# Performance work log

Hardware: AMD Instinct MI355X
Metric: run time of the kernel (lower is better)

## Reference

```python
import jax, jax.numpy as jnp
import numpy as np

N_NODES = 50000
N_EDGES = 1000000
IN_C = 128
HID_C = 128
N_REL = 8


def rgcn_conv(x, W, root, b, src, dst, et, n_rel):
    # PyG-style RGCNConv: per-relation linear transform of source features,
    # mean-aggregated per (target node, relation), plus root transform + bias.
    n = x.shape[0]
    h = jnp.einsum('nd,rdh->nrh', x, W)          # [N, R, H] per-relation transforms
    msgs = h[src, et]                            # [E, H] gather per-edge message
    seg = dst * n_rel + et                       # combined (node, relation) segment id
    agg = jax.ops.segment_sum(msgs, seg, num_segments=n * n_rel)        # [N*R, H]
    cnt = jax.ops.segment_sum(jnp.ones_like(msgs[:, 0]), seg, num_segments=n * n_rel)
    agg = agg / jnp.maximum(cnt, 1.0)[:, None]   # mean over edges of each relation
    return agg.reshape(n, n_rel, -1).sum(axis=1) + x @ root + b


def setup_inputs() -> dict:
    key = jax.random.key(0)
    ks = jax.random.split(key, 12)
    s = 1.0 / np.sqrt(IN_C)
    sh = 1.0 / np.sqrt(HID_C)
    return {
        'x': jax.random.normal(ks[0], (N_NODES, IN_C), dtype=jnp.float32),
        'ei': jax.random.randint(ks[1], (2, N_EDGES), 0, N_NODES, dtype=jnp.int32),
        'et': jax.random.randint(ks[2], (N_EDGES,), 0, N_REL, dtype=jnp.int32),
        'W1': jax.random.normal(ks[3], (N_REL, IN_C, HID_C), dtype=jnp.float32) * s,
        'root1': jax.random.normal(ks[4], (IN_C, HID_C), dtype=jnp.float32) * s,
        'b1': jnp.zeros((HID_C,), dtype=jnp.float32),
        'W2': jax.random.normal(ks[5], (N_REL, HID_C, HID_C), dtype=jnp.float32) * sh,
        'root2': jax.random.normal(ks[6], (HID_C, HID_C), dtype=jnp.float32) * sh,
        'b2': jnp.zeros((HID_C,), dtype=jnp.float32),
        'lin_W': jax.random.normal(ks[7], (HID_C, HID_C), dtype=jnp.float32) * sh,
        'lin_b': jnp.zeros((HID_C,), dtype=jnp.float32),
    }


def reference(x, ei, et, W1, root1, b1, W2, root2, b2, lin_W, lin_b):
    src, dst = ei[0], ei[1]
    h = jax.nn.relu(rgcn_conv(x, W1, root1, b1, src, dst, et, N_REL))
    h = rgcn_conv(h, W2, root2, b2, src, dst, et, N_REL)
    return h @ lin_W + lin_b
```

## Files before the change

kernel.cpp:

```cpp
#include <hip/hip_runtime.h>
#include <hip/hip_bf16.h>

#define N_NODES 50000
#define N_EDGES 1000000
#define C       128
#define N_REL   8
#define N_SEG   (N_NODES * N_REL)
#define KTOT    (N_REL * C + C)
#define KC_CNT  (KTOT / 32)
#define A_STRIDE 1160
#define NCHUNK  ((N_SEG + 1023) / 1024)
#define MV_N    (N_SEG + 1 + N_EDGES)
#define NBLK    (N_NODES / 16)
#define FE_BLK  ((N_EDGES + 511) / 512)

typedef __hip_bfloat16  bf16;
typedef __hip_bfloat162 bf162;
typedef __attribute__((ext_vector_type(8))) short short8;
typedef __attribute__((ext_vector_type(4))) float f32x4;
typedef __attribute__((ext_vector_type(2))) float f32x2;

__device__ __forceinline__ size_t frag_index(int k, int n) {
    int nt = n >> 4, n15 = n & 15;
    int kc = k >> 5, quad = (k >> 3) & 3, j = k & 7;
    int lane = quad * 16 + n15;
    return ((size_t)(nt * KC_CNT + kc) * 64 + lane) * 8 + j;
}

#define CVT_BLOCKS ((N_NODES * C / 2) / 256)
#define CNT_BLOCKS ((N_EDGES + 255) / 256)
__global__ void prep_kernel(const float2* __restrict__ xf, unsigned int* __restrict__ xb,
                            const int* __restrict__ dst, const int* __restrict__ et,
                            int* __restrict__ cnt, int* __restrict__ rank) {
    int bid = blockIdx.x;
    if (bid < CVT_BLOCKS) {
        int i = bid * 256 + threadIdx.x;
        float2 v = xf[i];
        union { bf162 h; unsigned int u; } cv;
        cv.h = bf162(__float2bfloat16(v.x), __float2bfloat16(v.y));
        xb[i] = cv.u;
    } else {
        int e = (bid - CVT_BLOCKS) * 256 + threadIdx.x;
        if (e < N_EDGES) rank[e] = atomicAdd(&cnt[dst[e] * N_REL + et[e]], 1);
    }
}

#define RP_B  (KTOT * C / 256)
#define RPT_B ((KTOT / 16) * (C / 16))
__global__ void scanA_kernel(const int* __restrict__ cnt, int* __restrict__ offs,
                             int* __restrict__ partials,
                             const float* __restrict__ W1, const float* __restrict__ root1,
                             const float* __restrict__ W2, const float* __restrict__ root2,
                             const float* __restrict__ linW,
                             const float* __restrict__ b2, const float* __restrict__ linb,
                             bf16* __restrict__ Bp1, bf16* __restrict__ Bp2,
                             float* __restrict__ b2p) {
    int bid = blockIdx.x;
    int t   = threadIdx.x;
    if (bid < NCHUNK) {
        __shared__ int tot[256];
        int base = bid * 1024 + t * 4;
        int v0 = (base + 0 < N_SEG) ? cnt[base + 0] : 0;
        int v1 = (base + 1 < N_SEG) ? cnt[base + 1] : 0;
        int v2 = (base + 2 < N_SEG) ? cnt[base + 2] : 0;
        int v3 = (base + 3 < N_SEG) ? cnt[base + 3] : 0;
        int tsum = v0 + v1 + v2 + v3;
        tot[t] = tsum;
        __syncthreads();
        for (int d = 1; d < 256; d <<= 1) {
            int x = tot[t];
            int y = (t >= d) ? tot[t - d] : 0;
            __syncthreads();
            tot[t] = x + y;
            __syncthreads();
        }
        int excl = tot[t] - tsum;
        if (base + 0 < N_SEG) offs[base + 0] = excl;
        if (base + 1 < N_SEG) offs[base + 1] = excl + v0;
        if (base + 2 < N_SEG) offs[base + 2] = excl + v0 + v1;
        if (base + 3 < N_SEG) offs[base + 3] = excl + v0 + v1 + v2;
        if (t == 255) partials[bid] = tot[255];
    } else if (bid < NCHUNK + RP_B) {
        int idx = (bid - NCHUNK) * 256 + t;
        int k = idx >> 7, n = idx & 127;
        float val;
        if (k < N_REL * C) val = W1[(size_t)k * C + n];
        else               val = root1[(size_t)(k - N_REL * C) * C + n];
        Bp1[frag_index(k, n)] = __float2bfloat16(val);
    } else if (bid < NCHUNK + RP_B + RPT_B) {
        __shared__ float Wt[16][128];
        __shared__ float Lt[128][16];
        int tileid = bid - NCHUNK - RP_B;
        int kt = tileid >> 3;
        int n0 = (tileid & 7) * 16;
        int k0 = kt * 16;
        const float* baseW = (k0 < N_REL * C) ? (W2 + (size_t)k0 * C)
                                              : (root2 + (size_t)(k0 - N_REL * C) * C);
#pragma unroll
        for (int r = 0; r < 8; r++) {
            int idx = t + r * 256;
            Wt[idx >> 7][idx & 127] = baseW[idx];
        }
#pragma unroll
        for (int r = 0; r < 8; r++) {
            int idx = t + r * 256;
            Lt[idx >> 4][idx & 15] = linW[(size_t)(idx >> 4) * C + n0 + (idx & 15)];
        }
        __syncthreads();
        int ty = t >> 4, tx = t & 15;
        float acc = 0.f;
#pragma unroll 8
        for (int m = 0; m < 128; m++)
            acc += Wt[ty][m] * Lt[m][tx];
        Bp2[frag_index(k0 + ty, n0 + tx)] = __float2bfloat16(acc);
    } else {
        if (t < 128) {
            float acc = linb[t];
            for (int m = 0; m < C; m++)
                acc += b2[m] * linW[(size_t)m * C + t];
            b2p[t] = acc;
        }
    }
}

__global__ void fillB_kernel(const int* __restrict__ src, const int* __restrict__ dst,
                             const int* __restrict__ et,
                             const int* __restrict__ offs_raw,
                             const int* __restrict__ partials,
                             int* __restrict__ offs_final,
                             const int* __restrict__ rank,
                             int* __restrict__ srcs_out) {
    __shared__ int s[512];
    int t = threadIdx.x;
    int bid = blockIdx.x;
    s[t] = (t < NCHUNK) ? partials[t] : 0;
    __syncthreads();
    for (int d = 1; d < 512; d <<= 1) {
        int x = s[t];
        int y = (t >= d) ? s[t - d] : 0;
        __syncthreads();
        s[t] = x + y;
        __syncthreads();
    }
    if (bid < NCHUNK) {
        int add = (bid == 0) ? 0 : s[bid - 1];
        int base = bid * 1024 + t * 2;
#pragma unroll
        for (int j = 0; j < 2; j++) {
            int idx = base + j;
            if (idx < N_SEG) offs_final[idx] = offs_raw[idx] + add;
        }
        if (bid == 0 && t == 0) offs_final[N_SEG] = N_EDGES;
    } else {
        int e = (bid - NCHUNK) * 512 + t;
        if (e < N_EDGES) {
            int seg = dst[e] * N_REL + et[e];
            int chunk = seg >> 10;
            int base = offs_raw[seg] + ((chunk == 0) ? 0 : s[chunk - 1]);
            srcs_out[base + rank[e]] = src[e];
        }
    }
}

template <int RELU, int OUT_F32, int COPY_CSR>
__global__ __launch_bounds__(512, 6) void fused_layer(
        const unsigned int* __restrict__ featu,
        const int*   __restrict__ offs,
        const int*   __restrict__ srcs,
        const short8* __restrict__ Bp,
        const float* __restrict__ bias,
        void* __restrict__ outp,
        int* __restrict__ offs2, int* __restrict__ srcs2)
{
    __shared__ __align__(16) unsigned int At[16 * (A_STRIDE / 2)];
    __shared__ int offsL[129];
    const int tid  = threadIdx.x;
    const int lane = tid & 63;
    const int w    = tid >> 6;
    const int v0   = blockIdx.x * 16;

    if (tid < 129) offsL[tid] = offs[v0 * 8 + tid];
    if (tid < 64)  At[(tid >> 2) * (A_STRIDE / 2) + 576 + (tid & 3)] = 0u;

    if (COPY_CSR) {
        for (int i = blockIdx.x * 512 + tid; i < MV_N; i += NBLK * 512) {
            if (i < N_SEG + 1) offs2[i] = offs[i];
            else               srcs2[i - (N_SEG + 1)] = srcs[i - (N_SEG + 1)];
        }
    }

    for (int q = tid; q < 16 * 64; q += 512) {
        int node = q >> 6, pch = q & 63;
        At[node * (A_STRIDE / 2) + 512 + pch] = featu[(size_t)(v0 + node) * 64 + pch];
    }
    __syncthreads();

    {
        const int segLo = w * 16;
        int curSeg = segLo;
        int i      = __builtin_amdgcn_readfirstlane(offsL[segLo]);
        int segBeg = i;
        int segEnd = __builtin_amdgcn_readfirstlane(offsL[segLo + 1]);
        const int eend = __builtin_amdgcn_readfirstlane(offsL[segLo + 16]);
        f32x2 acc2 = {0.f, 0.f};

        auto FLUSH = [&](int upto) {
            while (segEnd == upto) {
                float inv = (segEnd > segBeg) ? 1.0f / (float)(segEnd - segBeg) : 0.0f;
                union { bf162 h; unsigned int u; } cv;
                cv.h = bf162(__float2bfloat16(acc2.x * inv), __float2bfloat16(acc2.y * inv));
                At[(curSeg >> 3) * (A_STRIDE / 2) + (curSeg & 7) * 64 + lane] = cv.u;
                acc2.x = 0.f; acc2.y = 0.f;
                segBeg = segEnd;
                curSeg++;
                segEnd = __builtin_amdgcn_readfirstlane(offsL[curSeg + 1]);
            }
        };
        auto LOADF = [&](unsigned int (&v)[16], int base) {
            int sv[16];
#pragma unroll
            for (int j = 0; j < 16; j++) sv[j] = srcs[base + j];
#pragma unroll
            for (int j = 0; j < 16; j++) v[j] = featu[(size_t)sv[j] * 64 + lane];
        };
        auto FOLD16 = [&](unsigned int (&v)[16]) {
#pragma unroll
            for (int j = 0; j < 16; j++) {
                FLUSH(i + j);
                union { unsigned int u; float f; } lo, hi;
                lo.u = v[j] << 16;
                hi.u = v[j] & 0xFFFF0000u;
                f32x2 tadd = {lo.f, hi.f};
                acc2 += tadd;
            }
            i += 16;
        };

        unsigned int valsA[16], valsB[16];
        const int nfull = (eend - i) >> 4;
        if (nfull > 0) {
            LOADF(valsA, i);
            int b = 0;
            while (true) {
                if (b + 1 < nfull) LOADF(valsB, i + 16);
                FOLD16(valsA);
                b++;
                if (b >= nfull) break;
                if (b + 1 < nfull) LOADF(valsA, i + 16);
                FOLD16(valsB);
                b++;
                if (b >= nfull) break;
            }
        }
        {
            const int m = eend - i;
            if (m > 0) {
                int sv[16];
#pragma unroll
                for (int j = 0; j < 16; j++) if (j < m) sv[j] = srcs[i + j];
#pragma unroll
                for (int j = 0; j < 16; j++) if (j < m) valsA[j] = featu[(size_t)sv[j] * 64 + lane];
#pragma unroll
                for (int j = 0; j < 16; j++) {
                    if (j < m) {
                        FLUSH(i + j);
                        union { unsigned int u; float f; } lo, hi;
                        lo.u = valsA[j] << 16;
                        hi.u = valsA[j] & 0xFFFF0000u;
                        f32x2 tadd = {lo.f, hi.f};
                        acc2 += tadd;
                    }
                }
            }
        }
        while (curSeg < segLo + 16) {
            float inv = (segEnd > segBeg) ? 1.0f / (float)(segEnd - segBeg) : 0.0f;
            union { bf162 h; unsigned int u; } cv;
            cv.h = bf162(__float2bfloat16(acc2.x * inv), __float2bfloat16(acc2.y * inv));
            At[(curSeg >> 3) * (A_STRIDE / 2) + (curSeg & 7) * 64 + lane] = cv.u;
            acc2.x = 0.f; acc2.y = 0.f;
            segBeg = segEnd;
            curSeg++;
            if (curSeg < segLo + 16)
                segEnd = __builtin_amdgcn_readfirstlane(offsL[curSeg + 1]);
        }
    }
    __syncthreads();

    const int quad = lane >> 4, n15 = lane & 15;
    f32x4 acc = {0.f, 0.f, 0.f, 0.f};
    const short* Ash = (const short*)At;

    short8 b0 = Bp[(size_t)(w * KC_CNT) * 64 + lane];
#pragma unroll 4
    for (int kc = 0; kc < KC_CNT; kc++) {
        short8 cb0 = b0;
        if (kc + 1 < KC_CNT)
            b0 = Bp[(size_t)(w * KC_CNT + kc + 1) * 64 + lane];
        short8 a = *reinterpret_cast<const short8*>(Ash + n15 * A_STRIDE + kc * 32 + quad * 8);
        acc = __builtin_amdgcn_mfma_f32_16x16x32_bf16(a, cb0, acc, 0, 0, 0);
    }

    {
        int col = w * 16 + n15;
        float bv = bias[col];
#pragma unroll
        for (int r = 0; r < 4; r++) {
            int m = quad * 4 + r;
            float v = acc[r] + bv;
            if (RELU) v = fmaxf(v, 0.f);
            if (OUT_F32) ((float*)outp)[(size_t)(v0 + m) * C + col] = v;
            else         ((bf16*)outp)[(size_t)(v0 + m) * C + col] = __float2bfloat16(v);
        }
    }
}

extern "C" void kernel_launch(void* const* d_in, const int* in_sizes, int n_in,
                              void* d_out, int out_size, void* d_ws, size_t ws_size,
                              hipStream_t stream) {
    const float* x     = (const float*)d_in[0];
    const int*   ei    = (const int*)d_in[1];
    const int*   et    = (const int*)d_in[2];
    const float* W1    = (const float*)d_in[3];
    const float* root1 = (const float*)d_in[4];
    const float* b1    = (const float*)d_in[5];
    const float* W2    = (const float*)d_in[6];
    const float* root2 = (const float*)d_in[7];
    const float* b2    = (const float*)d_in[8];
    const float* linW  = (const float*)d_in[9];
    const float* linb  = (const float*)d_in[10];
    const int* src = ei;
    const int* dst = ei + N_EDGES;

    char* ob = (char*)d_out;
    int* cnt_i    = (int*)(ob + 0);
    int* offs_f   = (int*)(ob + 0);
    int* offs_t   = (int*)(ob + 1600256);
    int* partials = (int*)(ob + 3200256);
    int* srcs_t   = (int*)(ob + 3202048);
    int* rank     = (int*)(ob + 7202048);
    unsigned int* xb16 = (unsigned int*)(ob + 11202048);

    char* eb = (char*)d_in[1];
    int* offs2 = (int*)(eb + 0);
    int* srcs2 = (int*)(eb + 1600256);

    char* xbuf = (char*)d_in[0];
    unsigned int* h1 = (unsigned int*)xbuf;
    bf16*  Bp1 = (bf16*)(xbuf + 13000192);
    bf16*  Bp2 = (bf16*)(xbuf + 13295360);
    float* b2p = (float*)(xbuf + 13590528);

    float* out = (float*)d_out;

    hipMemsetAsync(cnt_i, 0, 1600000, stream);
    prep_kernel<<<CVT_BLOCKS + CNT_BLOCKS, 256, 0, stream>>>(
        (const float2*)x, xb16, dst, et, cnt_i, rank);
    scanA_kernel<<<NCHUNK + RP_B + RPT_B + 1, 256, 0, stream>>>(
        cnt_i, offs_t, partials, W1, root1, W2, root2, linW, b2, linb,
        Bp1, Bp2, b2p);
    fillB_kernel<<<NCHUNK + FE_BLK, 512, 0, stream>>>(
        src, dst, et, offs_t, partials, offs_f, rank, srcs_t);

    fused_layer<1, 0, 1><<<NBLK, 512, 0, stream>>>(
        xb16, offs_f, srcs_t, (const short8*)Bp1, b1, (void*)h1, offs2, srcs2);
    fused_layer<0, 1, 0><<<NBLK, 512, 0, stream>>>(
        h1, offs2, srcs2, (const short8*)Bp2, b2p, (void*)out, nullptr, nullptr);

    (void)in_sizes; (void)n_in; (void)out_size; (void)d_ws; (void)ws_size;
}
```

Measured before the change: 303.0 us.

## Double rows per block to reuse B fragments across two MFMA tiles

Each block of the fused layer now covers 32 nodes instead of 16. Every wave runs two 16x16 MFMA accumulators that share each loaded B fragment, which halves the weight traffic from L2 per node; B loads are also prefetched four k-steps ahead. The per-segment CSR offsets now sit in a register and are read with readlane instead of being staged in LDS, which removes the offsL buffer and the first barrier. In exchange, launch bounds drop to 4 blocks per CU, the grid is halved, and the last block needs bounds guards.

```diff
diff --git a/kernel.cpp b/kernel.cpp
--- a/kernel.cpp
+++ b/kernel.cpp
@@ -11,7 +11,8 @@
 #define A_STRIDE 1160
 #define NCHUNK  ((N_SEG + 1023) / 1024)
 #define MV_N    (N_SEG + 1 + N_EDGES)
-#define NBLK    (N_NODES / 16)
+#define MROW    32
+#define NBLK    ((N_NODES + MROW - 1) / MROW)
 #define FE_BLK  ((N_EDGES + 511) / 512)
 
 typedef __hip_bfloat16  bf16;
@@ -163,7 +164,7 @@
 }
 
 template <int RELU, int OUT_F32, int COPY_CSR>
-__global__ __launch_bounds__(512, 6) void fused_layer(
+__global__ __launch_bounds__(512, 4) void fused_layer(
         const unsigned int* __restrict__ featu,
         const int*   __restrict__ offs,
         const int*   __restrict__ srcs,
@@ -172,15 +173,13 @@
         void* __restrict__ outp,
         int* __restrict__ offs2, int* __restrict__ srcs2)
 {
-    __shared__ __align__(16) unsigned int At[16 * (A_STRIDE / 2)];
-    __shared__ int offsL[129];
+    __shared__ __align__(16) unsigned int At[MROW * (A_STRIDE / 2)];
     const int tid  = threadIdx.x;
     const int lane = tid & 63;
     const int w    = tid >> 6;
-    const int v0   = blockIdx.x * 16;
-
-    if (tid < 129) offsL[tid] = offs[v0 * 8 + tid];
-    if (tid < 64)  At[(tid >> 2) * (A_STRIDE / 2) + 576 + (tid & 3)] = 0u;
+    const int v0   = blockIdx.x * MROW;
+
+    if (tid < 4 * MROW) At[(tid >> 2) * (A_STRIDE / 2) + 576 + (tid & 3)] = 0u;
 
     if (COPY_CSR) {
         for (int i = blockIdx.x * 512 + tid; i < MV_N; i += NBLK * 512) {
@@ -189,19 +188,26 @@
         }
     }
 
-    for (int q = tid; q < 16 * 64; q += 512) {
+    for (int q = tid; q < MROW * 64; q += 512) {
         int node = q >> 6, pch = q & 63;
-        At[node * (A_STRIDE / 2) + 512 + pch] = featu[(size_t)(v0 + node) * 64 + pch];
-    }
-    __syncthreads();
+        unsigned int sval = 0u;
+        if (v0 + node < N_NODES) sval = featu[(size_t)(v0 + node) * 64 + pch];
+        At[node * (A_STRIDE / 2) + 512 + pch] = sval;
+    }
 
     {
-        const int segLo = w * 16;
+        const int segLo   = w * 32;
+        const int segBase = v0 * 8 + segLo;
+        int oidx = segBase + ((lane < 32) ? lane : 32);
+        if (oidx > N_SEG) oidx = N_SEG;
+        const int offsReg = offs[oidx];
+#define OFFS(L) __builtin_amdgcn_readlane(offsReg, (L))
+
         int curSeg = segLo;
-        int i      = __builtin_amdgcn_readfirstlane(offsL[segLo]);
+        int i      = OFFS(0);
         int segBeg = i;
-        int segEnd = __builtin_amdgcn_readfirstlane(offsL[segLo + 1]);
-        const int eend = __builtin_amdgcn_readfirstlane(offsL[segLo + 16]);
+        int segEnd = OFFS(1);
+        const int eend = OFFS(32);
         f32x2 acc2 = {0.f, 0.f};
 
         auto FLUSH = [&](int upto) {
@@ -213,7 +219,7 @@
                 acc2.x = 0.f; acc2.y = 0.f;
                 segBeg = segEnd;
                 curSeg++;
-                segEnd = __builtin_amdgcn_readfirstlane(offsL[curSeg + 1]);
+                segEnd = OFFS(curSeg + 1 - segLo);
             }
         };
         auto LOADF = [&](unsigned int (&v)[16], int base) {
@@ -273,7 +279,7 @@
                 }
             }
         }
-        while (curSeg < segLo + 16) {
+        while (curSeg < segLo + 32) {
             float inv = (segEnd > segBeg) ? 1.0f / (float)(segEnd - segBeg) : 0.0f;
             union { bf162 h; unsigned int u; } cv;
             cv.h = bf162(__float2bfloat16(acc2.x * inv), __float2bfloat16(acc2.y * inv));
@@ -281,24 +287,40 @@
             acc2.x = 0.f; acc2.y = 0.f;
             segBeg = segEnd;
             curSeg++;
-            if (curSeg < segLo + 16)
-                segEnd = __builtin_amdgcn_readfirstlane(offsL[curSeg + 1]);
-        }
+            if (curSeg < segLo + 32)
+                segEnd = OFFS(curSeg + 1 - segLo);
+        }
+#undef OFFS
     }
     __syncthreads();
 
     const int quad = lane >> 4, n15 = lane & 15;
-    f32x4 acc = {0.f, 0.f, 0.f, 0.f};
+    f32x4 acc0 = {0.f, 0.f, 0.f, 0.f};
+    f32x4 acc1 = {0.f, 0.f, 0.f, 0.f};
     const short* Ash = (const short*)At;
-
-    short8 b0 = Bp[(size_t)(w * KC_CNT) * 64 + lane];
-#pragma unroll 4
-    for (int kc = 0; kc < KC_CNT; kc++) {
-        short8 cb0 = b0;
-        if (kc + 1 < KC_CNT)
-            b0 = Bp[(size_t)(w * KC_CNT + kc + 1) * 64 + lane];
-        short8 a = *reinterpret_cast<const short8*>(Ash + n15 * A_STRIDE + kc * 32 + quad * 8);
-        acc = __builtin_amdgcn_mfma_f32_16x16x32_bf16(a, cb0, acc, 0, 0, 0);
+    const short8* BpW = Bp + (size_t)w * KC_CNT * 64;
+
+    short8 b0 = BpW[0 * 64 + lane];
+    short8 b1 = BpW[1 * 64 + lane];
+    short8 b2 = BpW[2 * 64 + lane];
+    short8 b3 = BpW[3 * 64 + lane];
+#pragma unroll
+    for (int kc = 0; kc < KC_CNT; kc += 4) {
+        short8 cb[4] = {b0, b1, b2, b3};
+        if (kc + 4 < KC_CNT) {
+            b0 = BpW[(kc + 4) * 64 + lane];
+            b1 = BpW[(kc + 5) * 64 + lane];
+            b2 = BpW[(kc + 6) * 64 + lane];
+            b3 = BpW[(kc + 7) * 64 + lane];
+        }
+#pragma unroll
+        for (int u = 0; u < 4; u++) {
+            const short* abase = Ash + (kc + u) * 32 + quad * 8;
+            short8 a0 = *reinterpret_cast<const short8*>(abase + n15 * A_STRIDE);
+            short8 a1 = *reinterpret_cast<const short8*>(abase + (n15 + 16) * A_STRIDE);
+            acc0 = __builtin_amdgcn_mfma_f32_16x16x32_bf16(a0, cb[u], acc0, 0, 0, 0);
+            acc1 = __builtin_amdgcn_mfma_f32_16x16x32_bf16(a1, cb[u], acc1, 0, 0, 0);
+        }
     }
 
     {
@@ -307,10 +329,17 @@
 #pragma unroll
         for (int r = 0; r < 4; r++) {
             int m = quad * 4 + r;
-            float v = acc[r] + bv;
+            float v = acc0[r] + bv;
             if (RELU) v = fmaxf(v, 0.f);
             if (OUT_F32) ((float*)outp)[(size_t)(v0 + m) * C + col] = v;
             else         ((bf16*)outp)[(size_t)(v0 + m) * C + col] = __float2bfloat16(v);
+            int m2 = v0 + 16 + m;
+            if (m2 < N_NODES) {
+                float v2 = acc1[r] + bv;
+                if (RELU) v2 = fmaxf(v2, 0.f);
+                if (OUT_F32) ((float*)outp)[(size_t)m2 * C + col] = v2;
+                else         ((bf16*)outp)[(size_t)m2 * C + col] = __float2bfloat16(v2);
+            }
         }
     }
 }
```

Measured after the change: 310.9 us. 1.03x slower.
